# Performance work log

Measured on AMD Instinct MI355X. Metric: run time of the kernel, lower is better.

Reference implementation:

```python
import jax, jax.numpy as jnp
import numpy as np

WIDTH = 1024
NUM_HEADS = 8
POWER = 8.0
MIN_RAD, MAX_RAD = 0.9, 0.999


def setup_inputs() -> dict:
    key = jax.random.key(0)
    k_x, k_a, k_wi, k_wa = jax.random.split(key, 4)
    B, L, W, H = 4, 8192, WIDTH, NUM_HEADS
    bw = W // H
    x = jax.random.normal(k_x, (B, L, W), dtype=jnp.float32)
    # a_param init, matching RGLRU.__init__
    unif = jax.random.uniform(k_a, shape=(W,))
    a_real = 0.5 * jnp.log(unif * (MAX_RAD**2 - MIN_RAD**2) + MIN_RAD**2 + 1e-08)
    a_param = jnp.log(jnp.exp(-a_real) - 1.0)
    scale = jnp.sqrt(1.0 / bw).astype(jnp.float32)
    w_in = jax.random.normal(k_wi, (H, bw, bw), dtype=jnp.float32) * scale
    b_in = jnp.zeros((H, bw), dtype=jnp.float32)
    w_a = jax.random.normal(k_wa, (H, bw, bw), dtype=jnp.float32) * scale
    b_a = jnp.zeros((H, bw), dtype=jnp.float32)
    return {"x": x, "a_param": a_param, "w_in": w_in, "b_in": b_in,
            "w_a": w_a, "b_a": b_a}


def _block_diag_linear(x, w, b):
    # x: [B, L, W]; w: [H, bw, bw]; b: [H, bw]
    B, L, W = x.shape
    H, bw, _ = w.shape
    xh = x.reshape(B, L, H, bw)
    y = jnp.einsum('blhi,hij->blhj', xh, w) + b
    return y.reshape(B, L, W)


def reference(x, a_param, w_in, b_in, w_a, b_a):
    gate_x = jax.nn.sigmoid(_block_diag_linear(x, w_in, b_in))
    gate_a = jax.nn.sigmoid(_block_diag_linear(x, w_a, b_a))
    log_a = -POWER * gate_a * jax.nn.softplus(a_param)          # [B, L, W]
    a = jnp.exp(log_a)
    a_squared = jnp.exp(2.0 * log_a)
    normalized_x = x * gate_x * jnp.sqrt(1.0 - a_squared)        # [B, L, W]

    h0 = jnp.zeros_like(normalized_x[:, 0, :])                   # [B, W]

    def step(h, inp):
        a_t, x_t = inp                                           # [B, W] each
        h = a_t * h + x_t
        return h, h

    # scan over time axis: move L to leading dim
    _, ys = jax.lax.scan(step, h0,
                         (jnp.swapaxes(a, 0, 1), jnp.swapaxes(normalized_x, 0, 1)))
    return jnp.swapaxes(ys, 0, 1)                                # [B, L, W]
```

## Files before the change

### kernel.cpp

```cpp
#include <hip/hip_runtime.h>
#include <math.h>

#define NB 4
#define NL 8192
#define NW 1024
#define NH 8
#define BWID 128
#define POWERF 8.0f

#define TM 64
#define NRC (NL / TM)
#define NCHAIN (NB * NH)
#define NBLK (NRC * NCHAIN)

typedef __attribute__((ext_vector_type(8))) short bf16x8;
typedef __attribute__((ext_vector_type(8))) unsigned short u16x8;
typedef __attribute__((ext_vector_type(4))) float f32x4;

__device__ __forceinline__ unsigned short bf_hi(float f) {
  return (unsigned short)(__float_as_uint(f) >> 16);
}
__device__ __forceinline__ float bf_f(unsigned short h) {
  return __uint_as_float(((unsigned)h) << 16);
}

__global__ void prep_kernel(const float* __restrict__ w_in,
                            const float* __restrict__ w_a,
                            const float* __restrict__ a_param,
                            unsigned short* __restrict__ wt,
                            float* __restrict__ sp,
                            unsigned long long* __restrict__ carry,
                            int* __restrict__ ticket) {
  const int gtid = blockIdx.x * 256 + threadIdx.x;
  const int k   = gtid & 127;
  const int col = (gtid >> 7) & 127;
  const int hh  = (gtid >> 14) & 7;
  const int mat = gtid >> 17;
  const float* src = mat ? w_a : w_in;
  const float v = src[((size_t)hh * 128 + k) * 128 + col];
  const unsigned short hi = bf_hi(v);
  const unsigned short lo = bf_hi(v - bf_f(hi));
  wt[(((size_t)(mat * 2 + 0) * 8 + hh) * 128 + col) * 128 + k] = hi;
  wt[(((size_t)(mat * 2 + 1) * 8 + hh) * 128 + col) * 128 + k] = lo;
  if (gtid < NW) sp[gtid] = log1pf(expf(a_param[gtid]));
  const size_t ci = (size_t)gtid * 4;
  carry[ci] = 0ull;
  carry[ci + 1] = 0ull;
  carry[ci + 2] = 0ull;
  carry[ci + 3] = 0ull;
  if (gtid == 0) *ticket = 0;
}

__global__ __launch_bounds__(256, 3)
void fused_kernel(const float* __restrict__ x,
                  const unsigned short* __restrict__ wt,
                  const float* __restrict__ sp,
                  const float* __restrict__ b_in,
                  const float* __restrict__ b_a,
                  float* __restrict__ out,
                  int* __restrict__ ticket,
                  unsigned long long* __restrict__ carry) {
  __shared__ char smem[49152];
  char* const pXh = smem;
  char* const pXl = smem + 16384;
  char* const pW  = smem + 32768;
  char* const pSeg = smem + 32768;

  const int tid  = threadIdx.x;
  if (tid == 0) *(int*)smem = atomicAdd(ticket, 1);
  __syncthreads();
  const int vbid = *(const int*)smem;
  __syncthreads();
  const int rc = vbid >> 5;
  const int bh = vbid & 31;
  const int b  = bh >> 3;
  const int h  = bh & 7;

  const int lane = tid & 63;
  const int wid  = tid >> 6;
  const int g  = lane >> 4;
  const int ln = lane & 15;
  const int wr = wid >> 1;
  const int wc = wid & 1;

  const size_t xbase = ((size_t)b * NL + (size_t)rc * TM) * NW + h * BWID;

  int wsoff[4], wdoff[4];
#pragma unroll
  for (int i = 0; i < 4; ++i) {
    const int chunk = tid + 256 * i;
    const int split = chunk >> 9;
    const int rem = chunk & 511;
    const int col = rem >> 2;
    const int kk8 = (rem & 3) * 8;
    wsoff[i] = split * 131072 + h * 16384 + col * 128 + kk8;
    wdoff[i] = col * 128 + ((split * 64 + kk8 * 2) ^ ((col & 7) << 4));
  }
  u16x8 wreg[4];
#pragma unroll
  for (int i = 0; i < 4; ++i) wreg[i] = *(const u16x8*)(wt + wsoff[i]);

#pragma unroll
  for (int i = 0; i < 4; ++i) {
    const int chunk = tid + 256 * i;
    const int row = chunk >> 4;
    const int k8  = (chunk & 15) * 8;
    const float4 v0 = *(const float4*)(x + xbase + (size_t)row * NW + k8);
    const float4 v1 = *(const float4*)(x + xbase + (size_t)row * NW + k8 + 4);
    const float f[8] = {v0.x, v0.y, v0.z, v0.w, v1.x, v1.y, v1.z, v1.w};
    u16x8 vh, vl;
#pragma unroll
    for (int j = 0; j < 8; ++j) {
      const unsigned short hi = bf_hi(f[j]);
      vh[j] = hi;
      vl[j] = bf_hi(f[j] - bf_f(hi));
    }
    const int off = row * 256 + ((k8 * 2) ^ ((row & 15) << 4));
    *(u16x8*)(pXh + off) = vh;
    *(u16x8*)(pXl + off) = vl;
  }
  __syncthreads();
#pragma unroll
  for (int i = 0; i < 4; ++i) *(u16x8*)(pW + wdoff[i]) = wreg[i];
#pragma unroll
  for (int i = 0; i < 4; ++i)
    wreg[i] = *(const u16x8*)(wt + wsoff[i] + 262144);

  f32x4 accx[2][4], acca[2][4];
#pragma unroll
  for (int rt = 0; rt < 2; ++rt)
#pragma unroll
    for (int ct = 0; ct < 4; ++ct) {
      accx[rt][ct] = (f32x4){0.f, 0.f, 0.f, 0.f};
      acca[rt][ct] = (f32x4){0.f, 0.f, 0.f, 0.f};
    }

  const int csw = (ln & 7) << 4;
  const int gk  = g * 16;

#pragma unroll 1
  for (int j = 0; j < 4; ++j) {
    const int kt = j * 32;
    __syncthreads();
    bf16x8 Ah[2], Al[2];
#pragma unroll
    for (int rt = 0; rt < 2; ++rt) {
      const int arow = wr * 32 + rt * 16 + ln;
      const int abyte = arow * 256 + (((kt + g * 8) * 2) ^ ((arow & 15) << 4));
      Ah[rt] = *(const bf16x8*)(pXh + abyte);
      Al[rt] = *(const bf16x8*)(pXl + abyte);
    }
#pragma unroll
    for (int ct = 0; ct < 4; ++ct) {
      const int cb = (wc * 64 + ct * 16 + ln) * 128;
      const bf16x8 Bh = *(const bf16x8*)(pW + cb + ((gk) ^ csw));
      const bf16x8 Bl = *(const bf16x8*)(pW + cb + ((64 + gk) ^ csw));
#pragma unroll
      for (int rt = 0; rt < 2; ++rt) {
        accx[rt][ct] = __builtin_amdgcn_mfma_f32_16x16x32_bf16(Ah[rt], Bh, accx[rt][ct], 0, 0, 0);
        accx[rt][ct] = __builtin_amdgcn_mfma_f32_16x16x32_bf16(Al[rt], Bh, accx[rt][ct], 0, 0, 0);
        accx[rt][ct] = __builtin_amdgcn_mfma_f32_16x16x32_bf16(Ah[rt], Bl, accx[rt][ct], 0, 0, 0);
      }
    }
    __syncthreads();
#pragma unroll
    for (int i = 0; i < 4; ++i) *(u16x8*)(pW + wdoff[i]) = wreg[i];
    if (j < 3) {
#pragma unroll
      for (int i = 0; i < 4; ++i)
        wreg[i] = *(const u16x8*)(wt + wsoff[i] + kt + 32);
    }
    __syncthreads();
#pragma unroll
    for (int ct = 0; ct < 4; ++ct) {
      const int cb = (wc * 64 + ct * 16 + ln) * 128;
      const bf16x8 Bh = *(const bf16x8*)(pW + cb + ((gk) ^ csw));
      const bf16x8 Bl = *(const bf16x8*)(pW + cb + ((64 + gk) ^ csw));
#pragma unroll
      for (int rt = 0; rt < 2; ++rt) {
        acca[rt][ct] = __builtin_amdgcn_mfma_f32_16x16x32_bf16(Ah[rt], Bh, acca[rt][ct], 0, 0, 0);
        acca[rt][ct] = __builtin_amdgcn_mfma_f32_16x16x32_bf16(Al[rt], Bh, acca[rt][ct], 0, 0, 0);
        acca[rt][ct] = __builtin_amdgcn_mfma_f32_16x16x32_bf16(Ah[rt], Bl, acca[rt][ct], 0, 0, 0);
      }
    }
    __syncthreads();
    if (j < 3) {
#pragma unroll
      for (int i = 0; i < 4; ++i) *(u16x8*)(pW + wdoff[i]) = wreg[i];
#pragma unroll
      for (int i = 0; i < 4; ++i)
        wreg[i] = *(const u16x8*)(wt + wsoff[i] + 262144 + kt + 32);
    }
  }

  float av_sav[2][4][4], xn_sav[2][4][4];
#pragma unroll
  for (int ct = 0; ct < 4; ++ct) {
    const int col = wc * 64 + ct * 16 + ln;
    const float bi  = b_in[h * BWID + col];
    const float ba  = b_a[h * BWID + col];
    const float spv = sp[h * BWID + col];
#pragma unroll
    for (int rt = 0; rt < 2; ++rt) {
#pragma unroll
      for (int r = 0; r < 4; ++r) {
        const int row = wr * 32 + rt * 16 + g * 4 + r;
        const float zx = accx[rt][ct][r] + bi;
        const float za = acca[rt][ct][r] + ba;
        const int xoff = row * 256 + ((col * 2) ^ ((row & 15) << 4));
        const float xv = bf_f(*(const unsigned short*)(pXh + xoff)) +
                         bf_f(*(const unsigned short*)(pXl + xoff));
        const float gx = __builtin_amdgcn_rcpf(1.f + __expf(-zx));
        const float ga = __builtin_amdgcn_rcpf(1.f + __expf(-za));
        const float la = -POWERF * ga * spv;
        const float av = __expf(la);
        const float asq = __expf(2.f * la);
        av_sav[rt][ct][r] = av;
        xn_sav[rt][ct][r] = xv * gx * sqrtf(fmaxf(1.f - asq, 0.f));
      }
    }
  }

#pragma unroll
  for (int ct = 0; ct < 4; ++ct) {
    const int col = wc * 64 + ct * 16 + ln;
#pragma unroll
    for (int rt = 0; rt < 2; ++rt) {
      float A4 = 1.f, h4 = 0.f;
#pragma unroll
      for (int r = 0; r < 4; ++r) {
        h4 = fmaf(av_sav[rt][ct][r], h4, xn_sav[rt][ct][r]);
        A4 *= av_sav[rt][ct][r];
      }
      const int s = wr * 8 + rt * 4 + g;
      *(float2*)(pSeg + col * 128 + ((s * 8) ^ ((col & 15) << 3))) =
          make_float2(A4, h4);
    }
  }
  __syncthreads();

  if (tid < 128) {
    const int w = tid;
    float As[16], hs[16];
#pragma unroll
    for (int s = 0; s < 16; ++s) {
      const float2 v =
          *(const float2*)(pSeg + w * 128 + ((s * 8) ^ ((w & 15) << 3)));
      As[s] = v.x;
      hs[s] = v.y;
    }
    float Atot = 1.f, hloc = 0.f;
#pragma unroll
    for (int s = 0; s < 16; ++s) {
      hloc = fmaf(As[s], hloc, hs[s]);
      Atot *= As[s];
    }
    const size_t cbase = ((size_t)vbid * 128 + w) * 2;
    __hip_atomic_store(carry + cbase + 1,
                       ((unsigned long long)__float_as_uint(-Atot) << 32) |
                           (unsigned long long)__float_as_uint(hloc),
                       __ATOMIC_RELAXED, __HIP_MEMORY_SCOPE_AGENT);

    float hprev = 0.f;
    if (rc > 0) {
      float P = 1.f, q = 0.f;
      int j = vbid - NCHAIN;
      int spins = 0;
      while (true) {
        const size_t jb = ((size_t)j * 128 + w) * 2;
        const unsigned long long wi = __hip_atomic_load(
            carry + jb, __ATOMIC_RELAXED, __HIP_MEMORY_SCOPE_AGENT);
        if (wi >> 32) {
          hprev = fmaf(P, __uint_as_float((unsigned)wi), q);
          break;
        }
        const unsigned long long wl = __hip_atomic_load(
            carry + jb + 1, __ATOMIC_RELAXED, __HIP_MEMORY_SCOPE_AGENT);
        if (wl >> 63) {
          const float Aj = -__uint_as_float((unsigned)(wl >> 32));
          const float hj = __uint_as_float((unsigned)wl);
          q = fmaf(P, hj, q);
          P *= Aj;
          if (j < NCHAIN) { hprev = q; break; }
          j -= NCHAIN;
          continue;
        }
        __builtin_amdgcn_s_sleep(1);
        if (++spins > (1 << 18)) { hprev = q; break; }
      }
    }
    const float Hm = fmaf(Atot, hprev, hloc);
    __hip_atomic_store(carry + cbase,
                       (1ull << 32) | (unsigned long long)__float_as_uint(Hm),
                       __ATOMIC_RELAXED, __HIP_MEMORY_SCOPE_AGENT);

    float p = hprev;
#pragma unroll
    for (int s = 0; s < 16; ++s) {
      *(float*)(pSeg + w * 128 + ((s * 8) ^ ((w & 15) << 3))) = p;
      p = fmaf(As[s], p, hs[s]);
    }
  }
  __syncthreads();

#pragma unroll
  for (int ct = 0; ct < 4; ++ct) {
    const int col = wc * 64 + ct * 16 + ln;
#pragma unroll
    for (int rt = 0; rt < 2; ++rt) {
      const int s = wr * 8 + rt * 4 + g;
      float hh =
          *(const float*)(pSeg + col * 128 + ((s * 8) ^ ((col & 15) << 3)));
#pragma unroll
      for (int r = 0; r < 4; ++r) {
        hh = fmaf(av_sav[rt][ct][r], hh, xn_sav[rt][ct][r]);
        out[xbase + (size_t)(wr * 32 + rt * 16 + g * 4 + r) * NW + col] = hh;
      }
    }
  }
}

extern "C" void kernel_launch(void* const* d_in, const int* in_sizes, int n_in,
                              void* d_out, int out_size, void* d_ws, size_t ws_size,
                              hipStream_t stream) {
  const float* x       = (const float*)d_in[0];
  const float* a_param = (const float*)d_in[1];
  const float* w_in    = (const float*)d_in[2];
  const float* b_in    = (const float*)d_in[3];
  const float* w_a     = (const float*)d_in[4];
  const float* b_a     = (const float*)d_in[5];
  float* out = (float*)d_out;

  char* ws = (char*)d_ws;
  unsigned long long* carry = (unsigned long long*)ws;
  int* ticket = (int*)(ws + (8 << 20));
  unsigned short* wt = (unsigned short*)(ws + (8 << 20) + 1024);
  float* sp = (float*)(ws + (8 << 20) + 1024 + (1 << 20));

  prep_kernel<<<1024, 256, 0, stream>>>(w_in, w_a, a_param, wt, sp,
                                        carry, ticket);
  fused_kernel<<<NBLK, 256, 0, stream>>>(x, wt, sp, b_in, b_a, out,
                                         ticket, carry);
}
```

Before: 299.0 us.

## Drop X staging in LDS, double-buffer weights, raise occupancy to four blocks

Removes the shared-memory staging of the split-bf16 X tile. Each lane now loads its MFMA A-fragment straight from global memory and converts it in registers, with the next K-slice prefetched. Weights are double-buffered in two LDS halves, which cuts barriers per stage, and total LDS drops from 48KB to 32KB so launch bounds can ask for 4 blocks per CU. In the epilogue x is re-read from global memory instead of LDS, and exp(2*la) is replaced by av*av, trading extra global traffic and register pressure for higher occupancy and fewer syncs.

```diff
diff --git a/kernel.cpp b/kernel.cpp
--- a/kernel.cpp
+++ b/kernel.cpp
@@ -51,7 +51,7 @@
   if (gtid == 0) *ticket = 0;
 }
 
-__global__ __launch_bounds__(256, 3)
+__global__ __launch_bounds__(256, 4)
 void fused_kernel(const float* __restrict__ x,
                   const unsigned short* __restrict__ wt,
                   const float* __restrict__ sp,
@@ -60,11 +60,10 @@
                   float* __restrict__ out,
                   int* __restrict__ ticket,
                   unsigned long long* __restrict__ carry) {
-  __shared__ char smem[49152];
-  char* const pXh = smem;
-  char* const pXl = smem + 16384;
-  char* const pW  = smem + 32768;
-  char* const pSeg = smem + 32768;
+  __shared__ char smem[32768];
+  char* const pW0 = smem;
+  char* const pW1 = smem + 16384;
+  char* const pSeg = smem;
 
   const int tid  = threadIdx.x;
   if (tid == 0) *(int*)smem = atomicAdd(ticket, 1);
@@ -96,32 +95,20 @@
     wsoff[i] = split * 131072 + h * 16384 + col * 128 + kk8;
     wdoff[i] = col * 128 + ((split * 64 + kk8 * 2) ^ ((col & 7) << 4));
   }
+
+  const float* const xr0 = x + xbase + (size_t)(wr * 32 + ln) * NW + g * 8;
+  const float* const xr1 = xr0 + 16 * NW;
+
   u16x8 wreg[4];
 #pragma unroll
   for (int i = 0; i < 4; ++i) wreg[i] = *(const u16x8*)(wt + wsoff[i]);
-
-#pragma unroll
-  for (int i = 0; i < 4; ++i) {
-    const int chunk = tid + 256 * i;
-    const int row = chunk >> 4;
-    const int k8  = (chunk & 15) * 8;
-    const float4 v0 = *(const float4*)(x + xbase + (size_t)row * NW + k8);
-    const float4 v1 = *(const float4*)(x + xbase + (size_t)row * NW + k8 + 4);
-    const float f[8] = {v0.x, v0.y, v0.z, v0.w, v1.x, v1.y, v1.z, v1.w};
-    u16x8 vh, vl;
-#pragma unroll
-    for (int j = 0; j < 8; ++j) {
-      const unsigned short hi = bf_hi(f[j]);
-      vh[j] = hi;
-      vl[j] = bf_hi(f[j] - bf_f(hi));
-    }
-    const int off = row * 256 + ((k8 * 2) ^ ((row & 15) << 4));
-    *(u16x8*)(pXh + off) = vh;
-    *(u16x8*)(pXl + off) = vl;
-  }
-  __syncthreads();
-#pragma unroll
-  for (int i = 0; i < 4; ++i) *(u16x8*)(pW + wdoff[i]) = wreg[i];
+  float4 xf[2][2];
+  xf[0][0] = *(const float4*)(xr0);
+  xf[0][1] = *(const float4*)(xr0 + 4);
+  xf[1][0] = *(const float4*)(xr1);
+  xf[1][1] = *(const float4*)(xr1 + 4);
+#pragma unroll
+  for (int i = 0; i < 4; ++i) *(u16x8*)(pW0 + wdoff[i]) = wreg[i];
 #pragma unroll
   for (int i = 0; i < 4; ++i)
     wreg[i] = *(const u16x8*)(wt + wsoff[i] + 262144);
@@ -137,59 +124,59 @@
 
   const int csw = (ln & 7) << 4;
   const int gk  = g * 16;
+  bf16x8 Ah[2], Al[2];
 
 #pragma unroll 1
-  for (int j = 0; j < 4; ++j) {
-    const int kt = j * 32;
+  for (int p = 0; p < 8; ++p) {
+    const int m = p & 1;
+    const int j = p >> 1;
     __syncthreads();
-    bf16x8 Ah[2], Al[2];
-#pragma unroll
-    for (int rt = 0; rt < 2; ++rt) {
-      const int arow = wr * 32 + rt * 16 + ln;
-      const int abyte = arow * 256 + (((kt + g * 8) * 2) ^ ((arow & 15) << 4));
-      Ah[rt] = *(const bf16x8*)(pXh + abyte);
-      Al[rt] = *(const bf16x8*)(pXl + abyte);
-    }
+    char* const pr = m ? pW1 : pW0;
+    char* const pw = m ? pW0 : pW1;
+    if (p < 7) {
+#pragma unroll
+      for (int i = 0; i < 4; ++i) *(u16x8*)(pw + wdoff[i]) = wreg[i];
+    }
+    if (p < 6) {
+      const int so = (((p + 2) & 1) ? 262144 : 0) + ((p + 2) >> 1) * 32;
+#pragma unroll
+      for (int i = 0; i < 4; ++i)
+        wreg[i] = *(const u16x8*)(wt + wsoff[i] + so);
+    }
+    if (m == 0) {
+#pragma unroll
+      for (int rt = 0; rt < 2; ++rt) {
+#pragma unroll
+        for (int q = 0; q < 2; ++q) {
+#pragma unroll
+          for (int e = 0; e < 4; ++e) {
+            const float f = xf[rt][q][e];
+            const unsigned short hi = bf_hi(f);
+            Ah[rt][q * 4 + e] = (short)hi;
+            Al[rt][q * 4 + e] = (short)bf_hi(f - bf_f(hi));
+          }
+        }
+      }
+      if (j < 3) {
+        const int ko = (j + 1) * 32;
+        xf[0][0] = *(const float4*)(xr0 + ko);
+        xf[0][1] = *(const float4*)(xr0 + ko + 4);
+        xf[1][0] = *(const float4*)(xr1 + ko);
+        xf[1][1] = *(const float4*)(xr1 + ko + 4);
+      }
+    }
+    f32x4* acc = m ? acca[0] : accx[0];
 #pragma unroll
     for (int ct = 0; ct < 4; ++ct) {
       const int cb = (wc * 64 + ct * 16 + ln) * 128;
-      const bf16x8 Bh = *(const bf16x8*)(pW + cb + ((gk) ^ csw));
-      const bf16x8 Bl = *(const bf16x8*)(pW + cb + ((64 + gk) ^ csw));
+      const bf16x8 Bh = *(const bf16x8*)(pr + cb + ((gk) ^ csw));
+      const bf16x8 Bl = *(const bf16x8*)(pr + cb + ((64 + gk) ^ csw));
 #pragma unroll
       for (int rt = 0; rt < 2; ++rt) {
-        accx[rt][ct] = __builtin_amdgcn_mfma_f32_16x16x32_bf16(Ah[rt], Bh, accx[rt][ct], 0, 0, 0);
-        accx[rt][ct] = __builtin_amdgcn_mfma_f32_16x16x32_bf16(Al[rt], Bh, accx[rt][ct], 0, 0, 0);
-        accx[rt][ct] = __builtin_amdgcn_mfma_f32_16x16x32_bf16(Ah[rt], Bl, accx[rt][ct], 0, 0, 0);
-      }
-    }
-    __syncthreads();
-#pragma unroll
-    for (int i = 0; i < 4; ++i) *(u16x8*)(pW + wdoff[i]) = wreg[i];
-    if (j < 3) {
-#pragma unroll
-      for (int i = 0; i < 4; ++i)
-        wreg[i] = *(const u16x8*)(wt + wsoff[i] + kt + 32);
-    }
-    __syncthreads();
-#pragma unroll
-    for (int ct = 0; ct < 4; ++ct) {
-      const int cb = (wc * 64 + ct * 16 + ln) * 128;
-      const bf16x8 Bh = *(const bf16x8*)(pW + cb + ((gk) ^ csw));
-      const bf16x8 Bl = *(const bf16x8*)(pW + cb + ((64 + gk) ^ csw));
-#pragma unroll
-      for (int rt = 0; rt < 2; ++rt) {
-        acca[rt][ct] = __builtin_amdgcn_mfma_f32_16x16x32_bf16(Ah[rt], Bh, acca[rt][ct], 0, 0, 0);
-        acca[rt][ct] = __builtin_amdgcn_mfma_f32_16x16x32_bf16(Al[rt], Bh, acca[rt][ct], 0, 0, 0);
-        acca[rt][ct] = __builtin_amdgcn_mfma_f32_16x16x32_bf16(Ah[rt], Bl, acca[rt][ct], 0, 0, 0);
-      }
-    }
-    __syncthreads();
-    if (j < 3) {
-#pragma unroll
-      for (int i = 0; i < 4; ++i) *(u16x8*)(pW + wdoff[i]) = wreg[i];
-#pragma unroll
-      for (int i = 0; i < 4; ++i)
-        wreg[i] = *(const u16x8*)(wt + wsoff[i] + 262144 + kt + 32);
+        acc[rt * 4 + ct] = __builtin_amdgcn_mfma_f32_16x16x32_bf16(Ah[rt], Bh, acc[rt * 4 + ct], 0, 0, 0);
+        acc[rt * 4 + ct] = __builtin_amdgcn_mfma_f32_16x16x32_bf16(Al[rt], Bh, acc[rt * 4 + ct], 0, 0, 0);
+        acc[rt * 4 + ct] = __builtin_amdgcn_mfma_f32_16x16x32_bf16(Ah[rt], Bl, acc[rt * 4 + ct], 0, 0, 0);
+      }
     }
   }
 
@@ -207,14 +194,12 @@
         const int row = wr * 32 + rt * 16 + g * 4 + r;
         const float zx = accx[rt][ct][r] + bi;
         const float za = acca[rt][ct][r] + ba;
-        const int xoff = row * 256 + ((col * 2) ^ ((row & 15) << 4));
-        const float xv = bf_f(*(const unsigned short*)(pXh + xoff)) +
-                         bf_f(*(const unsigned short*)(pXl + xoff));
+        const float xv = x[xbase + (size_t)row * NW + col];
         const float gx = __builtin_amdgcn_rcpf(1.f + __expf(-zx));
         const float ga = __builtin_amdgcn_rcpf(1.f + __expf(-za));
         const float la = -POWERF * ga * spv;
         const float av = __expf(la);
-        const float asq = __expf(2.f * la);
+        const float asq = av * av;
         av_sav[rt][ct][r] = av;
         xn_sav[rt][ct][r] = xv * gx * sqrtf(fmaxf(1.f - asq, 0.f));
       }
```

Result: slower. 761.7 us (+154.8%).
